# Kernel optimization log

Measured on AMD Instinct MI355X. Metric: run time of the kernel, lower is better.

The kernel has to match this reference:

```python
import jax, jax.numpy as jnp
import numpy as np

B, T, D = 128, 32, 1024
ADA, INTER, RANK = 1024, 1024, 8
LN_EPS = 1e-5

def setup_inputs() -> dict:
    key = jax.random.key(0)
    ks = jax.random.split(key, 9)
    return {
        "x": jax.random.normal(ks[0], (B, T, D), dtype=jnp.float32),
        "ada_emb": jax.random.normal(ks[1], (B, ADA), dtype=jnp.float32),
        "base_layer": jax.random.normal(ks[2], (D, D), dtype=jnp.float32),  # torch.randn init
        "w1": jax.random.normal(ks[3], (ADA, INTER), dtype=jnp.float32) * 0.02,
        "b1": jnp.zeros((INTER,), dtype=jnp.float32),
        "w2": jax.random.normal(ks[4], (INTER, 2 * D * RANK), dtype=jnp.float32) * 0.02,
        "b2": jnp.zeros((2 * D * RANK,), dtype=jnp.float32),
        "ln_g": jnp.ones((ADA,), dtype=jnp.float32),
        "ln_b": jnp.zeros((ADA,), dtype=jnp.float32),
    }

def _layernorm(x, g, b):
    mu = jnp.mean(x, axis=-1, keepdims=True)
    var = jnp.var(x, axis=-1, keepdims=True)
    return (x - mu) * jax.lax.rsqrt(var + LN_EPS) * g + b

def reference(x, ada_emb, base_layer, w1, b1, w2, b2, ln_g, ln_b):
    b, t, d = x.shape
    # hypernetwork: cond -> per-sample LoRA factors
    ae = _layernorm(ada_emb, ln_g, ln_b)
    h = jax.nn.gelu(ae @ w1 + b1, approximate=False)  # nn.GELU is exact (erf)
    xw = h @ w2 + b2                                   # (B, 2*D*rank)
    x_a, x_b = jnp.split(xw, 2, axis=-1)
    x_a = x_a.reshape(b, d, RANK)
    x_b = x_b.reshape(b, d, RANK)
    # fused per-sample weight: base + x_a @ x_b^T  -> (B, D, D)
    layer = base_layer[None, :, :] + jnp.einsum('bdr,bkr->bdk', x_a, x_b)
    # apply shared per-sample weight to every token (equiv to repeat_interleave + bmm)
    out = jnp.einsum('btc,bco->bto', x, layer)
    return x + out  # residual=True
```

## Files before the change

### kernel.cpp

```cpp
#include <hip/hip_runtime.h>
#include <hip/hip_bf16.h>
#include <math.h>

#define BB    128
#define TT    32
#define DD    1024
#define NADA  1024
#define NINT  1024
#define NRANK 8
#define LNEPS 1e-5f
#define TKCH  8
#define SPL2  8
#define SPLW  2
#define XWN   (2 * DD * NRANK)

using bf16x8 = __attribute__((ext_vector_type(8))) short;
using f32x4  = __attribute__((ext_vector_type(4))) float;

__device__ __forceinline__ short f2bf(float f) {
    __hip_bfloat16 h = __float2bfloat16(f);
    return *reinterpret_cast<short*>(&h);
}

__device__ __forceinline__ float bf2f(short s) {
    unsigned u = ((unsigned)(unsigned short)s) << 16;
    return __uint_as_float(u);
}

__device__ __forceinline__ void async16(const void* g, void* l) {
    __builtin_amdgcn_global_load_lds(
        (const __attribute__((address_space(1))) void*)g,
        (__attribute__((address_space(3))) void*)l, 16, 0, 0);
}

__device__ __forceinline__ void tcast_tile(
    const float* __restrict__ in, short* __restrict__ out, int K, int N,
    int bx, int by, bool addI, int tid, float (*t)[68])
{
    const int n0 = bx * 64, k0 = by * 64;
    #pragma unroll
    for (int it = 0; it < 4; ++it) {
        const int idx = it * 256 + tid;
        const int r = idx >> 4, c4 = (idx & 15) * 4;
        float4 v = *(const float4*)(in + (size_t)(k0 + r) * N + n0 + c4);
        t[r][c4 + 0] = v.x; t[r][c4 + 1] = v.y;
        t[r][c4 + 2] = v.z; t[r][c4 + 3] = v.w;
    }
    __syncthreads();
    #pragma unroll
    for (int it = 0; it < 4; ++it) {
        const int idx = it * 256 + tid;
        const int rn = idx >> 4, c4 = (idx & 15) * 4;
        float f0 = t[c4 + 0][rn], f1 = t[c4 + 1][rn];
        float f2 = t[c4 + 2][rn], f3 = t[c4 + 3][rn];
        if (addI) {
            const int n = n0 + rn;
            if (k0 + c4 + 0 == n) f0 += 1.f;
            if (k0 + c4 + 1 == n) f1 += 1.f;
            if (k0 + c4 + 2 == n) f2 += 1.f;
            if (k0 + c4 + 3 == n) f3 += 1.f;
        }
        short4 p;
        p.x = f2bf(f0); p.y = f2bf(f1); p.z = f2bf(f2); p.w = f2bf(f3);
        *(short4*)(out + (size_t)(n0 + rn) * K + k0 + c4) = p;
    }
}

__global__ __launch_bounds__(256) void prep_kernel(
    const float* __restrict__ x, const float* __restrict__ w1,
    const float* __restrict__ base, const float* __restrict__ ada,
    const float* __restrict__ lng, const float* __restrict__ lnb,
    short* __restrict__ x_bf, short* __restrict__ w1t,
    short* __restrict__ baset, short* __restrict__ ae_bf)
{
    __shared__ float t[64][68];
    const int bid = blockIdx.x, tid = threadIdx.x;

    if (bid < 2048) {
        const int i0 = bid * 512 + tid;
        float4 v0 = reinterpret_cast<const float4*>(x)[i0];
        float4 v1 = reinterpret_cast<const float4*>(x)[i0 + 256];
        short4 p0, p1;
        p0.x = f2bf(v0.x); p0.y = f2bf(v0.y); p0.z = f2bf(v0.z); p0.w = f2bf(v0.w);
        p1.x = f2bf(v1.x); p1.y = f2bf(v1.y); p1.z = f2bf(v1.z); p1.w = f2bf(v1.w);
        reinterpret_cast<short4*>(x_bf)[i0] = p0;
        reinterpret_cast<short4*>(x_bf)[i0 + 256] = p1;
    } else if (bid < 2304) {
        const int b = bid - 2048;
        tcast_tile(w1, w1t, NADA, NINT, b & 15, b >> 4, false, tid, t);
    } else if (bid < 2560) {
        const int b = bid - 2304;
        tcast_tile(base, baset, DD, DD, b & 15, b >> 4, true, tid, t);
    } else {
        const int b = bid - 2560;
        const float* row = ada + (size_t)b * NADA;
        float sum = 0.f, sumsq = 0.f;
        for (int i = tid; i < NADA; i += 256) {
            float v = row[i];
            sum += v; sumsq += v * v;
        }
        #pragma unroll
        for (int off = 32; off > 0; off >>= 1) {
            sum   += __shfl_down(sum, off);
            sumsq += __shfl_down(sumsq, off);
        }
        float* s1 = &t[0][0];
        float* s2 = &t[1][0];
        const int wid = tid >> 6, lane = tid & 63;
        if (lane == 0) { s1[wid] = sum; s2[wid] = sumsq; }
        __syncthreads();
        if (tid == 0) {
            float a = 0.f, c = 0.f;
            for (int i = 0; i < 4; ++i) { a += s1[i]; c += s2[i]; }
            s1[0] = a; s2[0] = c;
        }
        __syncthreads();
        const float mu  = s1[0] * (1.f / NADA);
        const float var = s2[0] * (1.f / NADA) - mu * mu;
        const float inv = rsqrtf(var + LNEPS);
        for (int i = tid; i < NADA; i += 256) {
            ae_bf[(size_t)b * NADA + i] = f2bf((row[i] - mu) * inv * lng[i] + lnb[i]);
        }
    }
}

template <int BM, int BN, int WM, int WN, int EPI>
__global__ __launch_bounds__(256, 2) void mgemm(
    const short* __restrict__ A, const short* __restrict__ Bt,
    float* __restrict__ C, int M, int N, int K, int kLen,
    const float* __restrict__ tp, const float* __restrict__ p3,
    const float* __restrict__ b2)
{
    constexpr int MT = BM / WM / 16;
    constexpr int NT = BN / WN / 16;
    constexpr int LA = BM / 64;
    constexpr int LB = BN / 64;

    __shared__ __align__(16) short As[BM * 64];
    __shared__ __align__(16) short Bs[BN * 64];
    __shared__ float tmS[(EPI == 2) ? BM * 8 : 1];
    __shared__ float xbS[(EPI == 2) ? (BM / 32) * BN * 8 : 1];

    const int bm = blockIdx.y * BM;
    const int bn = blockIdx.x * BN;
    const int kStart = blockIdx.z * kLen;
    const int tid = threadIdx.x;
    const int wave = tid >> 6, lane = tid & 63;
    const int wm0 = (wave / WN) * (BM / WM);
    const int wn0 = (wave % WN) * (BN / WN);
    const int quad = lane >> 4, r16 = lane & 15;

    if constexpr (EPI == 2) {
        float4 a = {0.f, 0.f, 0.f, 0.f};
        #pragma unroll
        for (int ch = 0; ch < TKCH; ++ch) {
            float4 v = *(const float4*)(tp + (size_t)ch * BB * TT * NRANK
                                           + (size_t)bm * 8 + tid * 4);
            a.x += v.x; a.y += v.y; a.z += v.z; a.w += v.w;
        }
        *(float4*)&tmS[tid * 4] = a;
        const int b0 = bm >> 5;
        const int grp = tid >> 6;
        const int inner = tid & 63;
        const size_t off = (size_t)(b0 + grp) * XWN + DD * NRANK + (size_t)bn * 8
                         + inner * 8;
        const int bcol = DD * NRANK + bn * 8 + inner * 8;
        float4 s0a = *(const float4*)(p3 + off);
        float4 s0b = *(const float4*)(p3 + off + 4);
        float4 s1a = *(const float4*)(p3 + (size_t)BB * XWN + off);
        float4 s1b = *(const float4*)(p3 + (size_t)BB * XWN + off + 4);
        float4 ba  = *(const float4*)(b2 + bcol);
        float4 bb  = *(const float4*)(b2 + bcol + 4);
        float4 r0 = {s0a.x + s1a.x + ba.x, s0a.y + s1a.y + ba.y,
                     s0a.z + s1a.z + ba.z, s0a.w + s1a.w + ba.w};
        float4 r1 = {s0b.x + s1b.x + bb.x, s0b.y + s1b.y + bb.y,
                     s0b.z + s1b.z + bb.z, s0b.w + s1b.w + bb.w};
        *(float4*)&xbS[grp * BN * 8 + inner * 8]     = r0;
        *(float4*)&xbS[grp * BN * 8 + inner * 8 + 4] = r1;
    }

    f32x4 acc[MT][NT] = {};

    for (int kt = 0; kt < kLen; kt += 64) {
        const int k0 = kStart + kt;
        #pragma unroll
        for (int kk = 0; kk < 2; ++kk) {
            #pragma unroll
            for (int s = 0; s < LA; ++s) {
                const int c = s * 256 + tid;
                async16(A + (size_t)(bm + (c >> 2)) * K + k0 + kk * 32 + (c & 3) * 8,
                        &As[kk * BM * 32 + c * 8]);
            }
            #pragma unroll
            for (int s = 0; s < LB; ++s) {
                const int c = s * 256 + tid;
                async16(Bt + (size_t)(bn + (c >> 2)) * K + k0 + kk * 32 + (c & 3) * 8,
                        &Bs[kk * BN * 32 + c * 8]);
            }
        }
        __syncthreads();
        #pragma unroll
        for (int kk = 0; kk < 2; ++kk) {
            bf16x8 af[MT], bfr[NT];
            #pragma unroll
            for (int i = 0; i < MT; ++i)
                af[i] = *reinterpret_cast<const bf16x8*>(
                    &As[kk * BM * 32 + (wm0 + i * 16 + r16) * 32 + quad * 8]);
            #pragma unroll
            for (int j = 0; j < NT; ++j)
                bfr[j] = *reinterpret_cast<const bf16x8*>(
                    &Bs[kk * BN * 32 + (wn0 + j * 16 + r16) * 32 + quad * 8]);
            #pragma unroll
            for (int i = 0; i < MT; ++i)
                #pragma unroll
                for (int j = 0; j < NT; ++j)
                    acc[i][j] = __builtin_amdgcn_mfma_f32_16x16x32_bf16(
                        af[i], bfr[j], acc[i][j], 0, 0, 0);
        }
        __syncthreads();
    }

    if constexpr (EPI == 2) {
        float xbr[NT][8];
        #pragma unroll
        for (int i = 0; i < MT; ++i) {
            const int mlBase = wm0 + i * 16 + quad * 4;
            const int s = mlBase >> 5;
            #pragma unroll
            for (int j = 0; j < NT; ++j) {
                const int nl = wn0 + j * 16 + r16;
                #pragma unroll
                for (int rr = 0; rr < 8; ++rr)
                    xbr[j][rr] = xbS[(s * BN + nl) * 8 + rr];
            }
            #pragma unroll
            for (int r = 0; r < 4; ++r) {
                const int ml = mlBase + r;
                const int m = bm + ml;
                float t8[8];
                #pragma unroll
                for (int rr = 0; rr < 8; ++rr) t8[rr] = tmS[ml * 8 + rr];
                #pragma unroll
                for (int j = 0; j < NT; ++j) {
                    const int n = bn + wn0 + j * 16 + r16;
                    float v = acc[i][j][r];
                    #pragma unroll
                    for (int rr = 0; rr < 8; ++rr) v += t8[rr] * xbr[j][rr];
                    C[(size_t)m * N + n] = v;
                }
            }
        }
    } else {
        #pragma unroll
        for (int i = 0; i < MT; ++i) {
            #pragma unroll
            for (int r = 0; r < 4; ++r) {
                const int m = bm + wm0 + i * 16 + quad * 4 + r;
                #pragma unroll
                for (int j = 0; j < NT; ++j) {
                    const int n = bn + wn0 + j * 16 + r16;
                    C[((size_t)blockIdx.z * M + m) * N + n] = acc[i][j][r];
                }
            }
        }
    }
}

template <int SPLITK>
__global__ __launch_bounds__(256, 2) void gemm_w2(
    const short* __restrict__ A, const float* __restrict__ W,
    float* __restrict__ P, int M, int N, int K)
{
    constexpr int BM = 128, BN = 64;
    constexpr int MT = 4, NT = 2;
    __shared__ __align__(16) short As[BM * 64];
    __shared__ __align__(16) float Bf[64 * BN];

    const int bn = blockIdx.x * BN;
    const int kLen = K / SPLITK;
    const int kStart = blockIdx.z * kLen;
    const int tid = threadIdx.x;
    const int wave = tid >> 6, lane = tid & 63;
    const int wm0 = (wave >> 1) * 64;
    const int wn0 = (wave & 1) * 32;
    const int quad = lane >> 4, r16 = lane & 15;

    f32x4 acc[MT][NT] = {};

    for (int kt = 0; kt < kLen; kt += 64) {
        const int k0 = kStart + kt;
        #pragma unroll
        for (int kk = 0; kk < 2; ++kk) {
            #pragma unroll
            for (int s = 0; s < 2; ++s) {
                const int c = s * 256 + tid;
                async16(A + (size_t)(c >> 2) * K + k0 + kk * 32 + (c & 3) * 8,
                        &As[kk * BM * 32 + c * 8]);
            }
            #pragma unroll
            for (int s = 0; s < 2; ++s) {
                const int c = s * 256 + tid;
                async16(W + (size_t)(k0 + kk * 32 + (c >> 4)) * N + bn + (c & 15) * 4,
                        &Bf[kk * 32 * BN + c * 4]);
            }
        }
        __syncthreads();
        #pragma unroll
        for (int kk = 0; kk < 2; ++kk) {
            bf16x8 af[MT], bfr[NT];
            #pragma unroll
            for (int i = 0; i < MT; ++i)
                af[i] = *reinterpret_cast<const bf16x8*>(
                    &As[kk * BM * 32 + (wm0 + i * 16 + r16) * 32 + quad * 8]);
            #pragma unroll
            for (int j = 0; j < NT; ++j) {
                const int n = wn0 + j * 16 + r16;
                short tmp[8];
                #pragma unroll
                for (int t = 0; t < 8; ++t)
                    tmp[t] = f2bf(Bf[kk * 32 * BN + (quad * 8 + t) * BN + n]);
                bfr[j] = *reinterpret_cast<const bf16x8*>(tmp);
            }
            #pragma unroll
            for (int i = 0; i < MT; ++i)
                #pragma unroll
                for (int j = 0; j < NT; ++j)
                    acc[i][j] = __builtin_amdgcn_mfma_f32_16x16x32_bf16(
                        af[i], bfr[j], acc[i][j], 0, 0, 0);
        }
        __syncthreads();
    }

    #pragma unroll
    for (int i = 0; i < MT; ++i) {
        #pragma unroll
        for (int r = 0; r < 4; ++r) {
            const int m = wm0 + i * 16 + quad * 4 + r;
            #pragma unroll
            for (int j = 0; j < NT; ++j) {
                const int n = bn + wn0 + j * 16 + r16;
                P[((size_t)blockIdx.z * M + m) * N + n] = acc[i][j][r];
            }
        }
    }
}

__global__ __launch_bounds__(256) void combine_gelu(
    const float* __restrict__ part, const float* __restrict__ b1,
    short* __restrict__ h)
{
    const int i4 = (blockIdx.x * 256 + threadIdx.x) * 4;
    float4 s = *(const float4*)(b1 + (i4 & (NINT - 1)));
    #pragma unroll
    for (int z = 0; z < SPL2; ++z) {
        float4 p = *(const float4*)(part + (size_t)z * BB * NINT + i4);
        s.x += p.x; s.y += p.y; s.z += p.z; s.w += p.w;
    }
    s.x = 0.5f * s.x * (1.f + erff(s.x * 0.70710678118654752f));
    s.y = 0.5f * s.y * (1.f + erff(s.y * 0.70710678118654752f));
    s.z = 0.5f * s.z * (1.f + erff(s.z * 0.70710678118654752f));
    s.w = 0.5f * s.w * (1.f + erff(s.w * 0.70710678118654752f));
    short4 o;
    o.x = f2bf(s.x); o.y = f2bf(s.y); o.z = f2bf(s.z); o.w = f2bf(s.w);
    *(short4*)(h + i4) = o;
}

__global__ __launch_bounds__(256) void tpart_kernel(
    const short* __restrict__ x_bf, const float* __restrict__ p3,
    const float* __restrict__ b2, float* __restrict__ tp)
{
    __shared__ float xa[(DD / TKCH) * NRANK];
    const int b = blockIdx.x, ch = blockIdx.y;
    const int col0 = ch * (DD / TKCH) * NRANK;
    const size_t off = (size_t)b * XWN + col0;
    {
        const int i4 = threadIdx.x * 4;
        float4 v0 = *(const float4*)(p3 + off + i4);
        float4 v1 = *(const float4*)(p3 + (size_t)BB * XWN + off + i4);
        float4 vb = *(const float4*)(b2 + col0 + i4);
        float4 r = {v0.x + v1.x + vb.x, v0.y + v1.y + vb.y,
                    v0.z + v1.z + vb.z, v0.w + v1.w + vb.w};
        *(float4*)(xa + i4) = r;
    }
    __syncthreads();
    const int m = threadIdx.x >> 3;
    const int r = threadIdx.x & 7;
    const short* xrow = x_bf + ((size_t)b * TT + m) * DD + ch * (DD / TKCH);
    float accv = 0.f;
    #pragma unroll 2
    for (int c = 0; c < DD / TKCH; c += 8) {
        bf16x8 xr = *(const bf16x8*)(xrow + c);
        #pragma unroll
        for (int u = 0; u < 8; ++u)
            accv += bf2f(xr[u]) * xa[(c + u) * NRANK + r];
    }
    tp[((size_t)ch * BB * TT + (size_t)b * TT + m) * NRANK + r] = accv;
}

extern "C" void kernel_launch(void* const* d_in, const int* in_sizes, int n_in,
                              void* d_out, int out_size, void* d_ws, size_t ws_size,
                              hipStream_t stream)
{
    const float* x    = (const float*)d_in[0];
    const float* ada  = (const float*)d_in[1];
    const float* base = (const float*)d_in[2];
    const float* w1   = (const float*)d_in[3];
    const float* b1   = (const float*)d_in[4];
    const float* w2   = (const float*)d_in[5];
    const float* b2   = (const float*)d_in[6];
    const float* lng  = (const float*)d_in[7];
    const float* lnb  = (const float*)d_in[8];
    float* out = (float*)d_out;

    char* w = (char*)d_ws;
    short* x_bf  = (short*)w;  w += (size_t)8 << 20;
    short* w1t   = (short*)w;  w += (size_t)2 << 20;
    short* baset = (short*)w;  w += (size_t)2 << 20;
    short* ae_bf = (short*)w;  w += (size_t)256 << 10;
    short* h_bf  = (short*)w;  w += (size_t)256 << 10;
    float* p3    = (float*)w;  w += (size_t)16 << 20;
    float* tp    = (float*)w;  w += (size_t)1 << 20;
    float* part  = (float*)w;

    prep_kernel<<<2688, 256, 0, stream>>>(
        x, w1, base, ada, lng, lnb, x_bf, w1t, baset, ae_bf);
    mgemm<64, 64, 2, 2, 0><<<dim3(NINT / 64, BB / 64, SPL2), 256, 0, stream>>>(
        ae_bf, w1t, part, BB, NINT, NADA, NADA / SPL2, nullptr, nullptr, nullptr);
    combine_gelu<<<BB * NINT / 1024, 256, 0, stream>>>(part, b1, h_bf);
    gemm_w2<SPLW><<<dim3(XWN / 64, 1, SPLW), 256, 0, stream>>>(
        h_bf, w2, p3, BB, XWN, NINT);
    tpart_kernel<<<dim3(BB, TKCH), 256, 0, stream>>>(x_bf, p3, b2, tp);
    mgemm<128, 64, 2, 2, 2><<<dim3(DD / 64, BB * TT / 128), 256, 0, stream>>>(
        x_bf, baset, out, BB * TT, DD, DD, DD, tp, p3, b2);
}
```

Measured before the change: 178.0 us.

## Fuse all stages into one cooperative persistent kernel with grid syncs

Replaces the six separate launches (prep, split-K w1 GEMM, GELU combine, split-K w2 GEMM, t-partials, final GEMM) with a single cooperative kernel of 512 blocks that separates phases with grid.sync. The w1 GEMM drops split-K and fuses bias plus GELU in its epilogue, and the w2 GEMM drops split-K and writes biased results directly. Independent casting work (x and base transpose) is spread across the idle blocks while the small w1 GEMM runs. This removes launch gaps and partial-sum round-trips to memory, in exchange for grid-wide barriers and less parallelism in the early GEMMs, where only 32 blocks do the w1 GEMM.

```diff
diff --git a/kernel.cpp b/kernel.cpp
--- a/kernel.cpp
+++ b/kernel.cpp
@@ -1,6 +1,9 @@
 #include <hip/hip_runtime.h>
+#include <hip/hip_cooperative_groups.h>
 #include <hip/hip_bf16.h>
 #include <math.h>
+
+namespace cg = cooperative_groups;
 
 #define BB    128
 #define TT    32
@@ -10,8 +13,6 @@
 #define NRANK 8
 #define LNEPS 1e-5f
 #define TKCH  8
-#define SPL2  8
-#define SPLW  2
 #define XWN   (2 * DD * NRANK)
 
 using bf16x8 = __attribute__((ext_vector_type(8))) short;
@@ -37,6 +38,7 @@
     const float* __restrict__ in, short* __restrict__ out, int K, int N,
     int bx, int by, bool addI, int tid, float (*t)[68])
 {
+    __syncthreads();
     const int n0 = bx * 64, k0 = by * 64;
     #pragma unroll
     for (int it = 0; it < 4; ++it) {
@@ -66,33 +68,41 @@
     }
 }
 
-__global__ __launch_bounds__(256) void prep_kernel(
-    const float* __restrict__ x, const float* __restrict__ w1,
-    const float* __restrict__ base, const float* __restrict__ ada,
-    const float* __restrict__ lng, const float* __restrict__ lnb,
+__device__ __forceinline__ void xcast_job(
+    int j, const float* __restrict__ x, short* __restrict__ x_bf, int tid)
+{
+    const int i0 = j * 512 + tid;
+    float4 v0 = reinterpret_cast<const float4*>(x)[i0];
+    float4 v1 = reinterpret_cast<const float4*>(x)[i0 + 256];
+    short4 p0, p1;
+    p0.x = f2bf(v0.x); p0.y = f2bf(v0.y); p0.z = f2bf(v0.z); p0.w = f2bf(v0.w);
+    p1.x = f2bf(v1.x); p1.y = f2bf(v1.y); p1.z = f2bf(v1.z); p1.w = f2bf(v1.w);
+    reinterpret_cast<short4*>(x_bf)[i0] = p0;
+    reinterpret_cast<short4*>(x_bf)[i0 + 256] = p1;
+}
+
+__global__ __launch_bounds__(256, 2) void mega(
+    const float* __restrict__ x, const float* __restrict__ ada,
+    const float* __restrict__ base, const float* __restrict__ w1,
+    const float* __restrict__ b1, const float* __restrict__ w2,
+    const float* __restrict__ b2, const float* __restrict__ lng,
+    const float* __restrict__ lnb, float* __restrict__ out,
     short* __restrict__ x_bf, short* __restrict__ w1t,
-    short* __restrict__ baset, short* __restrict__ ae_bf)
+    short* __restrict__ baset, short* __restrict__ ae_bf,
+    short* __restrict__ h_bf, float* __restrict__ xw,
+    float* __restrict__ tp)
 {
-    __shared__ float t[64][68];
+    __shared__ __align__(16) char smem[61440];
+    cg::grid_group grid = cg::this_grid();
     const int bid = blockIdx.x, tid = threadIdx.x;
-
-    if (bid < 2048) {
-        const int i0 = bid * 512 + tid;
-        float4 v0 = reinterpret_cast<const float4*>(x)[i0];
-        float4 v1 = reinterpret_cast<const float4*>(x)[i0 + 256];
-        short4 p0, p1;
-        p0.x = f2bf(v0.x); p0.y = f2bf(v0.y); p0.z = f2bf(v0.z); p0.w = f2bf(v0.w);
-        p1.x = f2bf(v1.x); p1.y = f2bf(v1.y); p1.z = f2bf(v1.z); p1.w = f2bf(v1.w);
-        reinterpret_cast<short4*>(x_bf)[i0] = p0;
-        reinterpret_cast<short4*>(x_bf)[i0 + 256] = p1;
-    } else if (bid < 2304) {
-        const int b = bid - 2048;
-        tcast_tile(w1, w1t, NADA, NINT, b & 15, b >> 4, false, tid, t);
-    } else if (bid < 2560) {
-        const int b = bid - 2304;
-        tcast_tile(base, baset, DD, DD, b & 15, b >> 4, true, tid, t);
-    } else {
-        const int b = bid - 2560;
+    const int wave = tid >> 6, lane = tid & 63;
+    const int quad = lane >> 4, r16 = lane & 15;
+    float (*tT)[68] = (float(*)[68])smem;
+
+    if (bid < 256) {
+        tcast_tile(w1, w1t, NADA, NINT, bid & 15, bid >> 4, false, tid, tT);
+    } else if (bid < 384) {
+        const int b = bid - 256;
         const float* row = ada + (size_t)b * NADA;
         float sum = 0.f, sumsq = 0.f;
         for (int i = tid; i < NADA; i += 256) {
@@ -104,10 +114,10 @@
             sum   += __shfl_down(sum, off);
             sumsq += __shfl_down(sumsq, off);
         }
-        float* s1 = &t[0][0];
-        float* s2 = &t[1][0];
-        const int wid = tid >> 6, lane = tid & 63;
-        if (lane == 0) { s1[wid] = sum; s2[wid] = sumsq; }
+        float* s1 = &tT[0][0];
+        float* s2 = &tT[1][0];
+        const int wid = tid >> 6;
+        if ((tid & 63) == 0) { s1[wid] = sum; s2[wid] = sumsq; }
         __syncthreads();
         if (tid == 0) {
             float a = 0.f, c = 0.f;
@@ -121,117 +131,268 @@
         for (int i = tid; i < NADA; i += 256) {
             ae_bf[(size_t)b * NADA + i] = f2bf((row[i] - mu) * inv * lng[i] + lnb[i]);
         }
-    }
-}
-
-template <int BM, int BN, int WM, int WN, int EPI>
-__global__ __launch_bounds__(256, 2) void mgemm(
-    const short* __restrict__ A, const short* __restrict__ Bt,
-    float* __restrict__ C, int M, int N, int K, int kLen,
-    const float* __restrict__ tp, const float* __restrict__ p3,
-    const float* __restrict__ b2)
-{
-    constexpr int MT = BM / WM / 16;
-    constexpr int NT = BN / WN / 16;
-    constexpr int LA = BM / 64;
-    constexpr int LB = BN / 64;
-
-    __shared__ __align__(16) short As[BM * 64];
-    __shared__ __align__(16) short Bs[BN * 64];
-    __shared__ float tmS[(EPI == 2) ? BM * 8 : 1];
-    __shared__ float xbS[(EPI == 2) ? (BM / 32) * BN * 8 : 1];
-
-    const int bm = blockIdx.y * BM;
-    const int bn = blockIdx.x * BN;
-    const int kStart = blockIdx.z * kLen;
-    const int tid = threadIdx.x;
-    const int wave = tid >> 6, lane = tid & 63;
-    const int wm0 = (wave / WN) * (BM / WM);
-    const int wn0 = (wave % WN) * (BN / WN);
-    const int quad = lane >> 4, r16 = lane & 15;
-
-    if constexpr (EPI == 2) {
-        float4 a = {0.f, 0.f, 0.f, 0.f};
+    } else {
+        xcast_job(bid - 384, x, x_bf, tid);
+    }
+    grid.sync();
+
+    if (bid < 32) {
+        short* As = (short*)smem;
+        short* Bs = (short*)(smem + 16384);
+        const int bn = (bid & 15) * 64, bm = (bid >> 4) * 64;
+        const int wm0 = (wave >> 1) * 32, wn0 = (wave & 1) * 32;
+        f32x4 acc[2][2] = {};
+        auto stage = [&](int buf, int k0) {
+            #pragma unroll
+            for (int kk = 0; kk < 2; ++kk) {
+                async16(ae_bf + (size_t)(bm + (tid >> 2)) * NADA + k0 + kk * 32 + (tid & 3) * 8,
+                        &As[buf * 4096 + kk * 2048 + tid * 8]);
+                async16(w1t + (size_t)(bn + (tid >> 2)) * NADA + k0 + kk * 32 + (tid & 3) * 8,
+                        &Bs[buf * 4096 + kk * 2048 + tid * 8]);
+            }
+        };
+        auto compute = [&](int buf) {
+            #pragma unroll
+            for (int kk = 0; kk < 2; ++kk) {
+                bf16x8 af[2], bfr[2];
+                #pragma unroll
+                for (int i = 0; i < 2; ++i)
+                    af[i] = *reinterpret_cast<const bf16x8*>(
+                        &As[buf * 4096 + kk * 2048 + (wm0 + i * 16 + r16) * 32 + quad * 8]);
+                #pragma unroll
+                for (int j = 0; j < 2; ++j)
+                    bfr[j] = *reinterpret_cast<const bf16x8*>(
+                        &Bs[buf * 4096 + kk * 2048 + (wn0 + j * 16 + r16) * 32 + quad * 8]);
+                #pragma unroll
+                for (int i = 0; i < 2; ++i)
+                    #pragma unroll
+                    for (int j = 0; j < 2; ++j)
+                        acc[i][j] = __builtin_amdgcn_mfma_f32_16x16x32_bf16(
+                            af[i], bfr[j], acc[i][j], 0, 0, 0);
+            }
+        };
+        stage(0, 0);
+        __syncthreads();
+        int cur = 0;
+        for (int kt = 64; kt < NADA; kt += 64) {
+            stage(cur ^ 1, kt);
+            compute(cur);
+            __syncthreads();
+            cur ^= 1;
+        }
+        compute(cur);
         #pragma unroll
-        for (int ch = 0; ch < TKCH; ++ch) {
-            float4 v = *(const float4*)(tp + (size_t)ch * BB * TT * NRANK
-                                           + (size_t)bm * 8 + tid * 4);
-            a.x += v.x; a.y += v.y; a.z += v.z; a.w += v.w;
-        }
-        *(float4*)&tmS[tid * 4] = a;
-        const int b0 = bm >> 5;
-        const int grp = tid >> 6;
-        const int inner = tid & 63;
-        const size_t off = (size_t)(b0 + grp) * XWN + DD * NRANK + (size_t)bn * 8
-                         + inner * 8;
-        const int bcol = DD * NRANK + bn * 8 + inner * 8;
-        float4 s0a = *(const float4*)(p3 + off);
-        float4 s0b = *(const float4*)(p3 + off + 4);
-        float4 s1a = *(const float4*)(p3 + (size_t)BB * XWN + off);
-        float4 s1b = *(const float4*)(p3 + (size_t)BB * XWN + off + 4);
-        float4 ba  = *(const float4*)(b2 + bcol);
-        float4 bb  = *(const float4*)(b2 + bcol + 4);
-        float4 r0 = {s0a.x + s1a.x + ba.x, s0a.y + s1a.y + ba.y,
-                     s0a.z + s1a.z + ba.z, s0a.w + s1a.w + ba.w};
-        float4 r1 = {s0b.x + s1b.x + bb.x, s0b.y + s1b.y + bb.y,
-                     s0b.z + s1b.z + bb.z, s0b.w + s1b.w + bb.w};
-        *(float4*)&xbS[grp * BN * 8 + inner * 8]     = r0;
-        *(float4*)&xbS[grp * BN * 8 + inner * 8 + 4] = r1;
-    }
-
-    f32x4 acc[MT][NT] = {};
-
-    for (int kt = 0; kt < kLen; kt += 64) {
-        const int k0 = kStart + kt;
+        for (int i = 0; i < 2; ++i) {
+            #pragma unroll
+            for (int r = 0; r < 4; ++r) {
+                const int m = bm + wm0 + i * 16 + quad * 4 + r;
+                #pragma unroll
+                for (int j = 0; j < 2; ++j) {
+                    const int n = bn + wn0 + j * 16 + r16;
+                    float v = acc[i][j][r] + b1[n];
+                    v = 0.5f * v * (1.f + erff(v * 0.70710678118654752f));
+                    h_bf[(size_t)m * NINT + n] = f2bf(v);
+                }
+            }
+        }
+    } else {
+        for (int it = 0; it < 5; ++it) {
+            const int jb = (bid - 32) + it * 480;
+            if (jb < 1920) {
+                xcast_job(128 + jb, x, x_bf, tid);
+            } else if (jb < 2176) {
+                const int bt = jb - 1920;
+                tcast_tile(base, baset, DD, DD, bt & 15, bt >> 4, true, tid, tT);
+            }
+        }
+    }
+    grid.sync();
+
+    {
+        short* As = (short*)smem;
+        float* Bf = (float*)(smem + 32768);
+        const int bn = bid * 32;
+        const int wm0 = wave * 32;
+        f32x4 acc[2][2] = {};
+        auto stage = [&](int buf, int k0) {
+            #pragma unroll
+            for (int kk = 0; kk < 2; ++kk) {
+                #pragma unroll
+                for (int s = 0; s < 2; ++s) {
+                    const int c = s * 256 + tid;
+                    async16(h_bf + (size_t)(c >> 2) * NINT + k0 + kk * 32 + (c & 3) * 8,
+                            &As[buf * 8192 + kk * 4096 + c * 8]);
+                }
+                async16(w2 + (size_t)(k0 + kk * 32 + (tid >> 3)) * XWN + bn + (tid & 7) * 4,
+                        &Bf[buf * 2048 + kk * 1024 + tid * 4]);
+            }
+        };
+        auto compute = [&](int buf) {
+            #pragma unroll
+            for (int kk = 0; kk < 2; ++kk) {
+                bf16x8 af[2], bfr[2];
+                #pragma unroll
+                for (int i = 0; i < 2; ++i)
+                    af[i] = *reinterpret_cast<const bf16x8*>(
+                        &As[buf * 8192 + kk * 4096 + (wm0 + i * 16 + r16) * 32 + quad * 8]);
+                #pragma unroll
+                for (int j = 0; j < 2; ++j) {
+                    const int n = j * 16 + r16;
+                    short tmp[8];
+                    #pragma unroll
+                    for (int t = 0; t < 8; ++t)
+                        tmp[t] = f2bf(Bf[buf * 2048 + kk * 1024 + (quad * 8 + t) * 32 + n]);
+                    bfr[j] = *reinterpret_cast<const bf16x8*>(tmp);
+                }
+                #pragma unroll
+                for (int i = 0; i < 2; ++i)
+                    #pragma unroll
+                    for (int j = 0; j < 2; ++j)
+                        acc[i][j] = __builtin_amdgcn_mfma_f32_16x16x32_bf16(
+                            af[i], bfr[j], acc[i][j], 0, 0, 0);
+            }
+        };
+        __syncthreads();
+        stage(0, 0);
+        __syncthreads();
+        int cur = 0;
+        for (int kt = 64; kt < NINT; kt += 64) {
+            stage(cur ^ 1, kt);
+            compute(cur);
+            __syncthreads();
+            cur ^= 1;
+        }
+        compute(cur);
         #pragma unroll
-        for (int kk = 0; kk < 2; ++kk) {
-            #pragma unroll
-            for (int s = 0; s < LA; ++s) {
-                const int c = s * 256 + tid;
-                async16(A + (size_t)(bm + (c >> 2)) * K + k0 + kk * 32 + (c & 3) * 8,
-                        &As[kk * BM * 32 + c * 8]);
-            }
-            #pragma unroll
-            for (int s = 0; s < LB; ++s) {
-                const int c = s * 256 + tid;
-                async16(Bt + (size_t)(bn + (c >> 2)) * K + k0 + kk * 32 + (c & 3) * 8,
-                        &Bs[kk * BN * 32 + c * 8]);
-            }
-        }
-        __syncthreads();
+        for (int i = 0; i < 2; ++i) {
+            #pragma unroll
+            for (int r = 0; r < 4; ++r) {
+                const int m = wm0 + i * 16 + quad * 4 + r;
+                #pragma unroll
+                for (int j = 0; j < 2; ++j) {
+                    const int n = bn + j * 16 + r16;
+                    xw[(size_t)m * XWN + n] = acc[i][j][r] + b2[n];
+                }
+            }
+        }
+    }
+    grid.sync();
+
+    {
+        float* xa = (float*)smem;
         #pragma unroll
-        for (int kk = 0; kk < 2; ++kk) {
-            bf16x8 af[MT], bfr[NT];
-            #pragma unroll
-            for (int i = 0; i < MT; ++i)
-                af[i] = *reinterpret_cast<const bf16x8*>(
-                    &As[kk * BM * 32 + (wm0 + i * 16 + r16) * 32 + quad * 8]);
-            #pragma unroll
-            for (int j = 0; j < NT; ++j)
-                bfr[j] = *reinterpret_cast<const bf16x8*>(
-                    &Bs[kk * BN * 32 + (wn0 + j * 16 + r16) * 32 + quad * 8]);
-            #pragma unroll
-            for (int i = 0; i < MT; ++i)
-                #pragma unroll
-                for (int j = 0; j < NT; ++j)
-                    acc[i][j] = __builtin_amdgcn_mfma_f32_16x16x32_bf16(
-                        af[i], bfr[j], acc[i][j], 0, 0, 0);
-        }
-        __syncthreads();
-    }
-
-    if constexpr (EPI == 2) {
-        float xbr[NT][8];
+        for (int it = 0; it < 2; ++it) {
+            const int j = it * 512 + bid;
+            const int b = j >> 3, ch = j & 7;
+            const int col0 = ch * (DD / TKCH) * NRANK;
+            __syncthreads();
+            {
+                const int i4 = tid * 4;
+                *(float4*)(xa + i4) = *(const float4*)(xw + (size_t)b * XWN + col0 + i4);
+            }
+            __syncthreads();
+            const int m = tid >> 3;
+            const int r = tid & 7;
+            const short* xrow = x_bf + ((size_t)b * TT + m) * DD + ch * (DD / TKCH);
+            float accv = 0.f;
+            #pragma unroll 2
+            for (int c = 0; c < DD / TKCH; c += 8) {
+                bf16x8 xr = *(const bf16x8*)(xrow + c);
+                #pragma unroll
+                for (int u = 0; u < 8; ++u)
+                    accv += bf2f(xr[u]) * xa[(c + u) * NRANK + r];
+            }
+            tp[((size_t)ch * BB * TT + (size_t)b * TT + m) * NRANK + r] = accv;
+        }
+    }
+    grid.sync();
+
+    {
+        short* As  = (short*)smem;
+        short* Bs  = (short*)(smem + 32768);
+        float* tmS = (float*)(smem + 49152);
+        float* xbS = (float*)(smem + 53248);
+        const int bn = (bid & 15) * 64;
+        const int bm = (bid >> 4) * 128;
+        const int wm0 = (wave >> 1) * 64, wn0 = (wave & 1) * 32;
+
+        __syncthreads();
+        {
+            float4 a = {0.f, 0.f, 0.f, 0.f};
+            #pragma unroll
+            for (int ch = 0; ch < TKCH; ++ch) {
+                float4 v = *(const float4*)(tp + (size_t)ch * BB * TT * NRANK
+                                               + (size_t)bm * 8 + tid * 4);
+                a.x += v.x; a.y += v.y; a.z += v.z; a.w += v.w;
+            }
+            *(float4*)&tmS[tid * 4] = a;
+            const int b0 = bm >> 5;
+            const int grp = tid >> 6;
+            const int inner = tid & 63;
+            const size_t off = (size_t)(b0 + grp) * XWN + DD * NRANK
+                             + (size_t)bn * 8 + inner * 8;
+            float4 r0 = *(const float4*)(xw + off);
+            float4 r1 = *(const float4*)(xw + off + 4);
+            *(float4*)&xbS[grp * 512 + inner * 8]     = r0;
+            *(float4*)&xbS[grp * 512 + inner * 8 + 4] = r1;
+        }
+
+        f32x4 acc[4][2] = {};
+        auto stage = [&](int buf, int k0) {
+            #pragma unroll
+            for (int kk = 0; kk < 2; ++kk) {
+                #pragma unroll
+                for (int s = 0; s < 2; ++s) {
+                    const int c = s * 256 + tid;
+                    async16(x_bf + (size_t)(bm + (c >> 2)) * DD + k0 + kk * 32 + (c & 3) * 8,
+                            &As[buf * 8192 + kk * 4096 + c * 8]);
+                }
+                async16(baset + (size_t)(bn + (tid >> 2)) * DD + k0 + kk * 32 + (tid & 3) * 8,
+                        &Bs[buf * 4096 + kk * 2048 + tid * 8]);
+            }
+        };
+        auto compute = [&](int buf) {
+            #pragma unroll
+            for (int kk = 0; kk < 2; ++kk) {
+                bf16x8 af[4], bfr[2];
+                #pragma unroll
+                for (int i = 0; i < 4; ++i)
+                    af[i] = *reinterpret_cast<const bf16x8*>(
+                        &As[buf * 8192 + kk * 4096 + (wm0 + i * 16 + r16) * 32 + quad * 8]);
+                #pragma unroll
+                for (int j = 0; j < 2; ++j)
+                    bfr[j] = *reinterpret_cast<const bf16x8*>(
+                        &Bs[buf * 4096 + kk * 2048 + (wn0 + j * 16 + r16) * 32 + quad * 8]);
+                #pragma unroll
+                for (int i = 0; i < 4; ++i)
+                    #pragma unroll
+                    for (int j = 0; j < 2; ++j)
+                        acc[i][j] = __builtin_amdgcn_mfma_f32_16x16x32_bf16(
+                            af[i], bfr[j], acc[i][j], 0, 0, 0);
+            }
+        };
+        stage(0, 0);
+        __syncthreads();
+        int cur = 0;
+        for (int kt = 64; kt < DD; kt += 64) {
+            stage(cur ^ 1, kt);
+            compute(cur);
+            __syncthreads();
+            cur ^= 1;
+        }
+        compute(cur);
+
+        float xbr[2][8];
         #pragma unroll
-        for (int i = 0; i < MT; ++i) {
+        for (int i = 0; i < 4; ++i) {
             const int mlBase = wm0 + i * 16 + quad * 4;
             const int s = mlBase >> 5;
             #pragma unroll
-            for (int j = 0; j < NT; ++j) {
+            for (int j = 0; j < 2; ++j) {
                 const int nl = wn0 + j * 16 + r16;
                 #pragma unroll
                 for (int rr = 0; rr < 8; ++rr)
-                    xbr[j][rr] = xbS[(s * BN + nl) * 8 + rr];
+                    xbr[j][rr] = xbS[(s * 64 + nl) * 8 + rr];
             }
             #pragma unroll
             for (int r = 0; r < 4; ++r) {
@@ -241,160 +402,16 @@
                 #pragma unroll
                 for (int rr = 0; rr < 8; ++rr) t8[rr] = tmS[ml * 8 + rr];
                 #pragma unroll
-                for (int j = 0; j < NT; ++j) {
+                for (int j = 0; j < 2; ++j) {
                     const int n = bn + wn0 + j * 16 + r16;
                     float v = acc[i][j][r];
                     #pragma unroll
                     for (int rr = 0; rr < 8; ++rr) v += t8[rr] * xbr[j][rr];
-                    C[(size_t)m * N + n] = v;
-                }
-            }
-        }
-    } else {
-        #pragma unroll
-        for (int i = 0; i < MT; ++i) {
-            #pragma unroll
-            for (int r = 0; r < 4; ++r) {
-                const int m = bm + wm0 + i * 16 + quad * 4 + r;
-                #pragma unroll
-                for (int j = 0; j < NT; ++j) {
-                    const int n = bn + wn0 + j * 16 + r16;
-                    C[((size_t)blockIdx.z * M + m) * N + n] = acc[i][j][r];
-                }
-            }
-        }
-    }
-}
-
-template <int SPLITK>
-__global__ __launch_bounds__(256, 2) void gemm_w2(
-    const short* __restrict__ A, const float* __restrict__ W,
-    float* __restrict__ P, int M, int N, int K)
-{
-    constexpr int BM = 128, BN = 64;
-    constexpr int MT = 4, NT = 2;
-    __shared__ __align__(16) short As[BM * 64];
-    __shared__ __align__(16) float Bf[64 * BN];
-
-    const int bn = blockIdx.x * BN;
-    const int kLen = K / SPLITK;
-    const int kStart = blockIdx.z * kLen;
-    const int tid = threadIdx.x;
-    const int wave = tid >> 6, lane = tid & 63;
-    const int wm0 = (wave >> 1) * 64;
-    const int wn0 = (wave & 1) * 32;
-    const int quad = lane >> 4, r16 = lane & 15;
-
-    f32x4 acc[MT][NT] = {};
-
-    for (int kt = 0; kt < kLen; kt += 64) {
-        const int k0 = kStart + kt;
-        #pragma unroll
-        for (int kk = 0; kk < 2; ++kk) {
-            #pragma unroll
-            for (int s = 0; s < 2; ++s) {
-                const int c = s * 256 + tid;
-                async16(A + (size_t)(c >> 2) * K + k0 + kk * 32 + (c & 3) * 8,
-                        &As[kk * BM * 32 + c * 8]);
-            }
-            #pragma unroll
-            for (int s = 0; s < 2; ++s) {
-                const int c = s * 256 + tid;
-                async16(W + (size_t)(k0 + kk * 32 + (c >> 4)) * N + bn + (c & 15) * 4,
-                        &Bf[kk * 32 * BN + c * 4]);
-            }
-        }
-        __syncthreads();
-        #pragma unroll
-        for (int kk = 0; kk < 2; ++kk) {
-            bf16x8 af[MT], bfr[NT];
-            #pragma unroll
-            for (int i = 0; i < MT; ++i)
-                af[i] = *reinterpret_cast<const bf16x8*>(
-                    &As[kk * BM * 32 + (wm0 + i * 16 + r16) * 32 + quad * 8]);
-            #pragma unroll
-            for (int j = 0; j < NT; ++j) {
-                const int n = wn0 + j * 16 + r16;
-                short tmp[8];
-                #pragma unroll
-                for (int t = 0; t < 8; ++t)
-                    tmp[t] = f2bf(Bf[kk * 32 * BN + (quad * 8 + t) * BN + n]);
-                bfr[j] = *reinterpret_cast<const bf16x8*>(tmp);
-            }
-            #pragma unroll
-            for (int i = 0; i < MT; ++i)
-                #pragma unroll
-                for (int j = 0; j < NT; ++j)
-                    acc[i][j] = __builtin_amdgcn_mfma_f32_16x16x32_bf16(
-                        af[i], bfr[j], acc[i][j], 0, 0, 0);
-        }
-        __syncthreads();
-    }
-
-    #pragma unroll
-    for (int i = 0; i < MT; ++i) {
-        #pragma unroll
-        for (int r = 0; r < 4; ++r) {
-            const int m = wm0 + i * 16 + quad * 4 + r;
-            #pragma unroll
-            for (int j = 0; j < NT; ++j) {
-                const int n = bn + wn0 + j * 16 + r16;
-                P[((size_t)blockIdx.z * M + m) * N + n] = acc[i][j][r];
-            }
-        }
-    }
-}
-
-__global__ __launch_bounds__(256) void combine_gelu(
-    const float* __restrict__ part, const float* __restrict__ b1,
-    short* __restrict__ h)
-{
-    const int i4 = (blockIdx.x * 256 + threadIdx.x) * 4;
-    float4 s = *(const float4*)(b1 + (i4 & (NINT - 1)));
-    #pragma unroll
-    for (int z = 0; z < SPL2; ++z) {
-        float4 p = *(const float4*)(part + (size_t)z * BB * NINT + i4);
-        s.x += p.x; s.y += p.y; s.z += p.z; s.w += p.w;
-    }
-    s.x = 0.5f * s.x * (1.f + erff(s.x * 0.70710678118654752f));
-    s.y = 0.5f * s.y * (1.f + erff(s.y * 0.70710678118654752f));
-    s.z = 0.5f * s.z * (1.f + erff(s.z * 0.70710678118654752f));
-    s.w = 0.5f * s.w * (1.f + erff(s.w * 0.70710678118654752f));
-    short4 o;
-    o.x = f2bf(s.x); o.y = f2bf(s.y); o.z = f2bf(s.z); o.w = f2bf(s.w);
-    *(short4*)(h + i4) = o;
-}
-
-__global__ __launch_bounds__(256) void tpart_kernel(
-    const short* __restrict__ x_bf, const float* __restrict__ p3,
-    const float* __restrict__ b2, float* __restrict__ tp)
-{
-    __shared__ float xa[(DD / TKCH) * NRANK];
-    const int b = blockIdx.x, ch = blockIdx.y;
-    const int col0 = ch * (DD / TKCH) * NRANK;
-    const size_t off = (size_t)b * XWN + col0;
-    {
-        const int i4 = threadIdx.x * 4;
-        float4 v0 = *(const float4*)(p3 + off + i4);
-        float4 v1 = *(const float4*)(p3 + (size_t)BB * XWN + off + i4);
-        float4 vb = *(const float4*)(b2 + col0 + i4);
-        float4 r = {v0.x + v1.x + vb.x, v0.y + v1.y + vb.y,
-                    v0.z + v1.z + vb.z, v0.w + v1.w + vb.w};
-        *(float4*)(xa + i4) = r;
-    }
-    __syncthreads();
-    const int m = threadIdx.x >> 3;
-    const int r = threadIdx.x & 7;
-    const short* xrow = x_bf + ((size_t)b * TT + m) * DD + ch * (DD / TKCH);
-    float accv = 0.f;
-    #pragma unroll 2
-    for (int c = 0; c < DD / TKCH; c += 8) {
-        bf16x8 xr = *(const bf16x8*)(xrow + c);
-        #pragma unroll
-        for (int u = 0; u < 8; ++u)
-            accv += bf2f(xr[u]) * xa[(c + u) * NRANK + r];
-    }
-    tp[((size_t)ch * BB * TT + (size_t)b * TT + m) * NRANK + r] = accv;
+                    out[(size_t)m * DD + n] = v;
+                }
+            }
+        }
+    }
 }
 
 extern "C" void kernel_launch(void* const* d_in, const int* in_sizes, int n_in,
@@ -418,18 +435,14 @@
     short* baset = (short*)w;  w += (size_t)2 << 20;
     short* ae_bf = (short*)w;  w += (size_t)256 << 10;
     short* h_bf  = (short*)w;  w += (size_t)256 << 10;
-    float* p3    = (float*)w;  w += (size_t)16 << 20;
-    float* tp    = (float*)w;  w += (size_t)1 << 20;
-    float* part  = (float*)w;
-
-    prep_kernel<<<2688, 256, 0, stream>>>(
-        x, w1, base, ada, lng, lnb, x_bf, w1t, baset, ae_bf);
-    mgemm<64, 64, 2, 2, 0><<<dim3(NINT / 64, BB / 64, SPL2), 256, 0, stream>>>(
-        ae_bf, w1t, part, BB, NINT, NADA, NADA / SPL2, nullptr, nullptr, nullptr);
-    combine_gelu<<<BB * NINT / 1024, 256, 0, stream>>>(part, b1, h_bf);
-    gemm_w2<SPLW><<<dim3(XWN / 64, 1, SPLW), 256, 0, stream>>>(
-        h_bf, w2, p3, BB, XWN, NINT);
-    tpart_kernel<<<dim3(BB, TKCH), 256, 0, stream>>>(x_bf, p3, b2, tp);
-    mgemm<128, 64, 2, 2, 2><<<dim3(DD / 64, BB * TT / 128), 256, 0, stream>>>(
-        x_bf, baset, out, BB * TT, DD, DD, DD, tp, p3, b2);
-}
+    float* xw    = (float*)w;  w += (size_t)8 << 20;
+    float* tp    = (float*)w;
+
+    void* args[] = {
+        (void*)&x, (void*)&ada, (void*)&base, (void*)&w1, (void*)&b1,
+        (void*)&w2, (void*)&b2, (void*)&lng, (void*)&lnb, (void*)&out,
+        (void*)&x_bf, (void*)&w1t, (void*)&baset, (void*)&ae_bf,
+        (void*)&h_bf, (void*)&xw, (void*)&tp
+    };
+    hipLaunchCooperativeKernel((void*)mega, dim3(512), dim3(256), args, 0, stream);
+}
```

Result: slower. 424.1 us (+138.3%).
